# Kernel tuning notes

Hardware: AMD Instinct MI355X
Metric: run time of the kernel (lower is better)

The kernel has to match this reference:

```python
import jax, jax.numpy as jnp
import numpy as np

KH, KW = 3, 3
SH, SW = 1, 1


def _same_padding(ih, iw):
    ph = max(KH - SH, 0) if ih % SH == 0 else max(KH - ih % SH, 0)
    pw = max(KW - SW, 0) if iw % SW == 0 else max(KW - iw % SW, 0)
    pl = pw // 2
    pr = pw - pl
    pt = ph // 2
    pb = ph - pt
    return pl, pr, pt, pb


def setup_inputs() -> dict:
    key = jax.random.key(0)
    x = jax.random.normal(key, (32, 3, 512, 512), dtype=jnp.float32)
    return {"x": x}


def reference(x) -> jnp.ndarray:
    B, C, ih, iw = x.shape
    pl, pr, pt, pb = _same_padding(ih, iw)
    # reflect pad spatial dims (matches F.pad mode='reflect')
    xp = jnp.pad(x, ((0, 0), (0, 0), (pt, pb), (pl, pr)), mode='reflect')
    oh = (ih + pt + pb - KH) // SH + 1
    ow = (iw + pl + pr - KW) // SW + 1
    # gather the KH*KW shifted views (fixed small loop over kernel taps)
    taps = [xp[:, :, i:i + SH * oh:SH, j:j + SW * ow:SW]
            for i in range(KH) for j in range(KW)]
    patches = jnp.stack(taps, axis=-1)  # [B, C, oh, ow, KH*KW]
    # odd window (9): median == middle order statistic, same as torch.median
    return jnp.sort(patches, axis=-1)[..., (KH * KW) // 2]
```

## Files before the change

### kernel.cpp

```cpp
#include <hip/hip_runtime.h>


#define IMG_H 512
#define IMG_W 512
#define NXCD 8

__device__ __forceinline__ float min3f(float a, float b, float c) {
    return fminf(fminf(a, b), c);
}
__device__ __forceinline__ float max3f(float a, float b, float c) {
    return fmaxf(fmaxf(a, b), c);
}
__device__ __forceinline__ float med3f(float a, float b, float c) {
    return __builtin_amdgcn_fmed3f(a, b, c);
}

__global__ __launch_bounds__(256) void median3x3_kernel(
        const float* __restrict__ in, float* __restrict__ out,
        int nplanes, int blocks_per_xcd) {
    int bid = (int)blockIdx.x;
    int sbid = (bid & (NXCD - 1)) * blocks_per_xcd + (bid >> 3);

    const int lane = threadIdx.x & 63;
    const int stripe = sbid * 4 + (threadIdx.x >> 6);
    const int plane = stripe >> 8;
    const int y0 = (stripe & 255) * 2;
    const int x0 = lane * 8;
    if (plane >= nplanes) return;

    const size_t pbase = (size_t)plane * IMG_H * IMG_W;
    const float* bp = in + pbase;

    int ys[4];
    ys[0] = (y0 == 0) ? 1 : y0 - 1;
    ys[1] = y0;
    ys[2] = y0 + 1;
    ys[3] = (y0 + 2 == IMG_H) ? IMG_H - 2 : y0 + 2;

    float4 v0[4], v1[4];
#pragma unroll
    for (int k = 0; k < 4; ++k) {
        const float* r = bp + (size_t)ys[k] * IMG_W + x0;
        v0[k] = *reinterpret_cast<const float4*>(r);
        v1[k] = *reinterpret_cast<const float4*>(r + 4);
    }

    float L[4], R[4];
#pragma unroll
    for (int k = 0; k < 4; ++k) {
        float l  = __shfl_up(v1[k].w, 1);
        float rr = __shfl_down(v0[k].x, 1);
        L[k] = (lane == 0)  ? v0[k].y : l;
        R[k] = (lane == 63) ? v1[k].z : rr;
    }

    float* op = out + pbase + (size_t)y0 * IMG_W + x0;
#pragma unroll
    for (int w = 0; w < 2; ++w) {
        const float A[10] = {L[w],      v0[w].x,   v0[w].y,   v0[w].z,   v0[w].w,
                             v1[w].x,   v1[w].y,   v1[w].z,   v1[w].w,   R[w]};
        const float B[10] = {L[w+1],    v0[w+1].x, v0[w+1].y, v0[w+1].z, v0[w+1].w,
                             v1[w+1].x, v1[w+1].y, v1[w+1].z, v1[w+1].w, R[w+1]};
        const float C[10] = {L[w+2],    v0[w+2].x, v0[w+2].y, v0[w+2].z, v0[w+2].w,
                             v1[w+2].x, v1[w+2].y, v1[w+2].z, v1[w+2].w, R[w+2]};

        float lo[10], mi[10], hi[10];
#pragma unroll
        for (int i = 0; i < 10; ++i) {
            lo[i] = min3f(A[i], B[i], C[i]);
            mi[i] = med3f(A[i], B[i], C[i]);
            hi[i] = max3f(A[i], B[i], C[i]);
        }
        float o[8];
#pragma unroll
        for (int i = 0; i < 8; ++i) {
            o[i] = med3f(max3f(lo[i], lo[i + 1], lo[i + 2]),
                         med3f(mi[i], mi[i + 1], mi[i + 2]),
                         min3f(hi[i], hi[i + 1], hi[i + 2]));
        }
        *reinterpret_cast<float4*>(op + (size_t)w * IMG_W)
            = make_float4(o[0], o[1], o[2], o[3]);
        *reinterpret_cast<float4*>(op + (size_t)w * IMG_W + 4)
            = make_float4(o[4], o[5], o[6], o[7]);
    }
}

extern "C" void kernel_launch(void* const* d_in, const int* in_sizes, int n_in,
                              void* d_out, int out_size, void* d_ws, size_t ws_size,
                              hipStream_t stream) {
    const float* x = (const float*)d_in[0];
    float* out = (float*)d_out;
    int nplanes = in_sizes[0] / (IMG_H * IMG_W);

    int stripes = nplanes * (IMG_H / 2);
    int grid = stripes / 4;
    int blocks_per_xcd = grid / NXCD;
    median3x3_kernel<<<grid, 256, 0, stream>>>(x, out, nplanes, blocks_per_xcd);
}
```

Measured before the change: 34.75 us.

## Process eight output rows per wave with rolling row buffer

Each wave now computes an 8-row stripe instead of 2 rows. Input rows rotate through a 4-slot register ring, and the next row is loaded after each output row is stored. This cuts redundant halo reads from 2x to 1.25x and overlaps loads with compute. The cost is fewer blocks, which lowers parallelism, plus a longer serial per-thread chain.

```diff
diff --git a/kernel.cpp b/kernel.cpp
--- a/kernel.cpp
+++ b/kernel.cpp
@@ -4,6 +4,7 @@
 #define IMG_H 512
 #define IMG_W 512
 #define NXCD 8
+#define ROWS 8
 
 __device__ __forceinline__ float min3f(float a, float b, float c) {
     return fminf(fminf(a, b), c);
@@ -23,46 +24,53 @@
 
     const int lane = threadIdx.x & 63;
     const int stripe = sbid * 4 + (threadIdx.x >> 6);
-    const int plane = stripe >> 8;
-    const int y0 = (stripe & 255) * 2;
+    const int plane = stripe >> 6;
+    const int y0 = (stripe & 63) * ROWS;
     const int x0 = lane * 8;
     if (plane >= nplanes) return;
 
     const size_t pbase = (size_t)plane * IMG_H * IMG_W;
     const float* bp = in + pbase;
 
-    int ys[4];
-    ys[0] = (y0 == 0) ? 1 : y0 - 1;
-    ys[1] = y0;
-    ys[2] = y0 + 1;
-    ys[3] = (y0 + 2 == IMG_H) ? IMG_H - 2 : y0 + 2;
+    float4 va[4], vb[4];
+    float  Ls[4], Rs[4];
 
-    float4 v0[4], v1[4];
-#pragma unroll
-    for (int k = 0; k < 4; ++k) {
-        const float* r = bp + (size_t)ys[k] * IMG_W + x0;
-        v0[k] = *reinterpret_cast<const float4*>(r);
-        v1[k] = *reinterpret_cast<const float4*>(r + 4);
-    }
+#define LOADROW(slot, yy)                                                    \
+    do {                                                                     \
+        const float* _r = bp + (size_t)(yy) * IMG_W + x0;                    \
+        va[slot] = *reinterpret_cast<const float4*>(_r);                     \
+        vb[slot] = *reinterpret_cast<const float4*>(_r + 4);                 \
+    } while (0)
 
-    float L[4], R[4];
-#pragma unroll
-    for (int k = 0; k < 4; ++k) {
-        float l  = __shfl_up(v1[k].w, 1);
-        float rr = __shfl_down(v0[k].x, 1);
-        L[k] = (lane == 0)  ? v0[k].y : l;
-        R[k] = (lane == 63) ? v1[k].z : rr;
-    }
+#define EDGES(slot)                                                          \
+    do {                                                                     \
+        float _l = __shfl_up(vb[slot].w, 1);                                 \
+        float _r = __shfl_down(va[slot].x, 1);                               \
+        Ls[slot] = (lane == 0)  ? va[slot].y : _l;    \
+        Rs[slot] = (lane == 63) ? vb[slot].z : _r;   \
+    } while (0)
+
+    int ytop = (y0 == 0) ? 1 : y0 - 1;
+    LOADROW(0, ytop);
+    LOADROW(1, y0);
+    LOADROW(2, y0 + 1);
+    LOADROW(3, y0 + 2);
+    EDGES(0); EDGES(1); EDGES(2);
 
     float* op = out + pbase + (size_t)y0 * IMG_W + x0;
+
 #pragma unroll
-    for (int w = 0; w < 2; ++w) {
-        const float A[10] = {L[w],      v0[w].x,   v0[w].y,   v0[w].z,   v0[w].w,
-                             v1[w].x,   v1[w].y,   v1[w].z,   v1[w].w,   R[w]};
-        const float B[10] = {L[w+1],    v0[w+1].x, v0[w+1].y, v0[w+1].z, v0[w+1].w,
-                             v1[w+1].x, v1[w+1].y, v1[w+1].z, v1[w+1].w, R[w+1]};
-        const float C[10] = {L[w+2],    v0[w+2].x, v0[w+2].y, v0[w+2].z, v0[w+2].w,
-                             v1[w+2].x, v1[w+2].y, v1[w+2].z, v1[w+2].w, R[w+2]};
+    for (int t = 0; t < ROWS; ++t) {
+        const int sA = t & 3, sB = (t + 1) & 3, sC = (t + 2) & 3;
+
+        if (t >= 1) EDGES(sC);
+
+        const float A[10] = {Ls[sA], va[sA].x, va[sA].y, va[sA].z, va[sA].w,
+                             vb[sA].x, vb[sA].y, vb[sA].z, vb[sA].w, Rs[sA]};
+        const float B[10] = {Ls[sB], va[sB].x, va[sB].y, va[sB].z, va[sB].w,
+                             vb[sB].x, vb[sB].y, vb[sB].z, vb[sB].w, Rs[sB]};
+        const float C[10] = {Ls[sC], va[sC].x, va[sC].y, va[sC].z, va[sC].w,
+                             vb[sC].x, vb[sC].y, vb[sC].z, vb[sC].w, Rs[sC]};
 
         float lo[10], mi[10], hi[10];
 #pragma unroll
@@ -78,11 +86,19 @@
                          med3f(mi[i], mi[i + 1], mi[i + 2]),
                          min3f(hi[i], hi[i + 1], hi[i + 2]));
         }
-        *reinterpret_cast<float4*>(op + (size_t)w * IMG_W)
+        *reinterpret_cast<float4*>(op + (size_t)t * IMG_W)
             = make_float4(o[0], o[1], o[2], o[3]);
-        *reinterpret_cast<float4*>(op + (size_t)w * IMG_W + 4)
+        *reinterpret_cast<float4*>(op + (size_t)t * IMG_W + 4)
             = make_float4(o[4], o[5], o[6], o[7]);
+
+        if (t < ROWS - 2) {
+            int yn = y0 + t + 3;
+            yn = (yn == IMG_H) ? IMG_H - 2 : yn;
+            LOADROW(sA, yn);
+        }
     }
+#undef LOADROW
+#undef EDGES
 }
 
 extern "C" void kernel_launch(void* const* d_in, const int* in_sizes, int n_in,
@@ -92,7 +108,7 @@
     float* out = (float*)d_out;
     int nplanes = in_sizes[0] / (IMG_H * IMG_W);
 
-    int stripes = nplanes * (IMG_H / 2);
+    int stripes = nplanes * (IMG_H / ROWS);
     int grid = stripes / 4;
     int blocks_per_xcd = grid / NXCD;
     median3x3_kernel<<<grid, 256, 0, stream>>>(x, out, nplanes, blocks_per_xcd);
```

After: 38.02 us. 9.4% more time.
